# Kernel optimization log

Hardware: AMD Instinct MI355X
Metric: run time of the kernel (lower is better)

The kernel has to match this reference:

```python
import jax, jax.numpy as jnp
import numpy as np

B, S, D, H = 32, 2048, 128, 16  # batch, cached kv len, head dim (=d_model), heads
EPS = 1e-5


def setup_inputs() -> dict:
    key = jax.random.key(0)
    ks = jax.random.split(key, 5)
    d_total = D * H
    x = jax.random.normal(ks[0], (B, 1, D), jnp.float32)
    past_k = jax.random.normal(ks[1], (B, H, S, D), jnp.float32)
    past_v = jax.random.normal(ks[2], (B, H, S, D), jnp.float32)
    Wqkv = jax.random.normal(ks[3], (3 * d_total, D), jnp.float32) * 0.02
    bqkv = jnp.zeros((3 * d_total,), jnp.float32)
    Wout = jax.random.normal(ks[4], (D, d_total), jnp.float32) * 0.02
    bout = jnp.zeros((D,), jnp.float32)
    return {"x": x, "past_k": past_k, "past_v": past_v,
            "Wqkv": Wqkv, "bqkv": bqkv, "Wout": Wout, "bout": bout}


def reference(x, past_k, past_v, Wqkv, bqkv, Wout, bout):
    # QKV projection: (B,1,D) -> (B,1,3*H*D)
    qkv = x @ Wqkv.T + bqkv
    qkv = qkv.reshape(B, 1, 3 * H, D).transpose(0, 2, 1, 3)  # (B,3H,1,D)
    q, k_new, v_new = jnp.split(qkv, 3, axis=1)              # each (B,H,1,D)
    k = jnp.concatenate([past_k, k_new], axis=2)             # (B,H,S+1,D)
    v = jnp.concatenate([past_v, v_new], axis=2)
    # single-query attention (causal mask is trivially all-visible for q_len=1)
    scale = 1.0 / jnp.sqrt(jnp.float32(D))
    scores = jnp.einsum('bhqd,bhkd->bhqk', q, k) * scale     # (B,H,1,S+1)
    probs = jax.nn.softmax(scores, axis=-1)
    y = jnp.einsum('bhqk,bhkd->bhqd', probs, v)              # (B,H,1,D)
    y = y.transpose(0, 2, 1, 3).reshape(B, 1, H * D)         # (B,1,H*D)
    y = y @ Wout.T + bout                                    # (B,1,D)
    y = y + x                                                # residual
    # layer norm over last dim, no affine params
    mu = jnp.mean(y, axis=-1, keepdims=True)
    var = jnp.mean(jnp.square(y - mu), axis=-1, keepdims=True)
    out = (y - mu) / jnp.sqrt(var + EPS)
    return (out, k, v)
```

## Files before the change

### kernel.cpp

```cpp
#include <hip/hip_runtime.h>
#include <math.h>

#define B 32
#define S 2048
#define S1 2049
#define D 128
#define H 16
#define DT 2048
#define NS 4
#define ROWS_PER_SPLIT 512
#define EPS 1e-5f
#define SCALE 0.08838834764831845f

typedef float f4v __attribute__((ext_vector_type(4)));

__global__ void __launch_bounds__(256)
qkv_proj_kernel(const float* __restrict__ x,
                const float* __restrict__ Wqkv,
                const float* __restrict__ bqkv,
                float* __restrict__ qkv,
                float* __restrict__ out_k,
                float* __restrict__ out_v) {
    const int b = blockIdx.x;
    const int j = blockIdx.y * 256 + threadIdx.x;
    __shared__ float xs[D];
    if (threadIdx.x < D) xs[threadIdx.x] = x[b * D + threadIdx.x];
    __syncthreads();
    const float* w = Wqkv + (size_t)j * D;
    float acc = bqkv[j];
#pragma unroll
    for (int d = 0; d < D; d += 4) {
        float4 w4 = *reinterpret_cast<const float4*>(w + d);
        acc = fmaf(w4.x, xs[d + 0], acc);
        acc = fmaf(w4.y, xs[d + 1], acc);
        acc = fmaf(w4.z, xs[d + 2], acc);
        acc = fmaf(w4.w, xs[d + 3], acc);
    }
    qkv[(size_t)b * (3 * DT) + j] = acc;

    if (j >= DT) {
        const int r = j - DT;
        const int which = r >> 11;
        const int hd = r & (DT - 1);
        const int h = hd >> 7;
        const int d = hd & 127;
        float* dst = which ? out_v : out_k;
        dst[((size_t)(b * H + h) * S1 + S) * D + d] = acc;
    }
}

__global__ void __launch_bounds__(256)
attn_kernel(const float* __restrict__ past_k,
            const float* __restrict__ past_v,
            const float* __restrict__ qkv,
            float* __restrict__ out_k,
            float* __restrict__ out_v,
            float* __restrict__ part_ml,
            float* __restrict__ part_acc) {
    const int bx = blockIdx.x;
    const int split = bx & (NS - 1);
    const int bh = bx >> 2;
    const int b = bh >> 4;
    const int h = bh & (H - 1);
    const int tid  = threadIdx.x;
    const int wave = tid >> 6;
    const int lane = tid & 63;
    const int half = lane >> 5;
    const int l32  = lane & 31;
    const int rg   = wave * 2 + half;

    const f4v* __restrict__ kin  = (const f4v*)past_k + (size_t)(b * H + h) * S * 32;
    const f4v* __restrict__ vin  = (const f4v*)past_v + (size_t)(b * H + h) * S * 32;
    f4v* __restrict__ kout = (f4v*)out_k + (size_t)(b * H + h) * S1 * 32;
    f4v* __restrict__ vout = (f4v*)out_v + (size_t)(b * H + h) * S1 * 32;

    const f4v q4 = ((const f4v*)qkv)[(size_t)b * (3 * DT / 4) + h * 32 + l32];

    const int s0 = split * ROWS_PER_SPLIT + rg;

    float m = -1e30f;
    float l = 0.f;
    f4v acc = (f4v){0.f, 0.f, 0.f, 0.f};

#pragma unroll 4
    for (int it = 0; it < ROWS_PER_SPLIT / 8; ++it) {
        const int s = s0 + it * 8;
        const size_t off = (size_t)s * 32 + l32;
        f4v k4 = __builtin_nontemporal_load(&kin[off]);
        __builtin_nontemporal_store(k4, &kout[off]);
        f4v t = k4 * q4;
        float p = t.x + t.y + t.z + t.w;
        p += __shfl_xor(p, 1);
        p += __shfl_xor(p, 2);
        p += __shfl_xor(p, 4);
        p += __shfl_xor(p, 8);
        p += __shfl_xor(p, 16);
        p *= SCALE;
        f4v v4 = __builtin_nontemporal_load(&vin[off]);
        __builtin_nontemporal_store(v4, &vout[off]);
        const float mn = fmaxf(m, p);
        const float c = __expf(m - mn);
        const float e = __expf(p - mn);
        l = l * c + e;
        acc = acc * c;
        acc += v4 * e;
        m = mn;
    }

    __shared__ float sm[8];
    __shared__ float sl[8];
    __shared__ float sacc[8 * D];
    ((f4v*)sacc)[rg * 32 + l32] = acc;
    if (l32 == 0) { sm[rg] = m; sl[rg] = l; }
    __syncthreads();

    if (tid < D) {
        float M = sm[0];
#pragma unroll
        for (int g = 1; g < 8; ++g) M = fmaxf(M, sm[g]);
        float L = 0.f, y = 0.f;
#pragma unroll
        for (int g = 0; g < 8; ++g) {
            const float wgt = __expf(sm[g] - M);
            L += wgt * sl[g];
            y = fmaf(wgt, sacc[g * D + tid], y);
        }
        part_acc[(size_t)bx * D + tid] = y;
        if (tid == 0) {
            part_ml[2 * bx + 0] = M;
            part_ml[2 * bx + 1] = L;
        }
    }
}

__global__ void __launch_bounds__(1024)
out_proj_kernel(const float* __restrict__ x,
                const float* __restrict__ qkv,
                const float* __restrict__ part_ml,
                const float* __restrict__ part_acc,
                const float* __restrict__ Wout,
                const float* __restrict__ bout,
                float* __restrict__ out) {
    const int b = blockIdx.x;
    const int t = threadIdx.x;
    __shared__ float ys[DT];
    __shared__ float pp[D * 8];
    __shared__ float tb[D];

    {
        const int h = t >> 6;
        const int lane = t & 63;
        const float* qp   = qkv + (size_t)b * (3 * DT) + h * D;
        const float* knew = qp + DT;
        const float* vnew = qp + 2 * DT;
        float pd = qp[2 * lane] * knew[2 * lane] + qp[2 * lane + 1] * knew[2 * lane + 1];
        pd += __shfl_xor(pd, 1);
        pd += __shfl_xor(pd, 2);
        pd += __shfl_xor(pd, 4);
        pd += __shfl_xor(pd, 8);
        pd += __shfl_xor(pd, 16);
        pd += __shfl_xor(pd, 32);
        const float s = pd * SCALE;

        const int bh = b * H + h;
        float m0 = part_ml[2 * (bh * NS + 0)], l0 = part_ml[2 * (bh * NS + 0) + 1];
        float m1 = part_ml[2 * (bh * NS + 1)], l1 = part_ml[2 * (bh * NS + 1) + 1];
        float m2 = part_ml[2 * (bh * NS + 2)], l2 = part_ml[2 * (bh * NS + 2) + 1];
        float m3 = part_ml[2 * (bh * NS + 3)], l3 = part_ml[2 * (bh * NS + 3) + 1];
        float M = fmaxf(fmaxf(fmaxf(m0, m1), fmaxf(m2, m3)), s);
        const float w0 = __expf(m0 - M), w1 = __expf(m1 - M);
        const float w2 = __expf(m2 - M), w3 = __expf(m3 - M);
        const float wn = __expf(s - M);
        const float L = w0 * l0 + w1 * l1 + w2 * l2 + w3 * l3 + wn;
        const float invL = 1.0f / L;
#pragma unroll
        for (int r = 0; r < 2; ++r) {
            const int d = lane + r * 64;
            float y = wn * vnew[d];
            y = fmaf(w0, part_acc[(size_t)(bh * NS + 0) * D + d], y);
            y = fmaf(w1, part_acc[(size_t)(bh * NS + 1) * D + d], y);
            y = fmaf(w2, part_acc[(size_t)(bh * NS + 2) * D + d], y);
            y = fmaf(w3, part_acc[(size_t)(bh * NS + 3) * D + d], y);
            ys[h * D + d] = y * invL;
        }
    }
    __syncthreads();

    {
        const int d = t >> 3;
        const int sub = t & 7;
        const float* w = Wout + (size_t)d * DT + sub * 256;
        const float* y = ys + sub * 256;
        float acc = 0.f;
#pragma unroll
        for (int j = 0; j < 256; j += 4) {
            float4 w4 = *reinterpret_cast<const float4*>(w + j);
            acc = fmaf(w4.x, y[j + 0], acc);
            acc = fmaf(w4.y, y[j + 1], acc);
            acc = fmaf(w4.z, y[j + 2], acc);
            acc = fmaf(w4.w, y[j + 3], acc);
        }
        pp[d * 8 + sub] = acc;
    }
    __syncthreads();

    float val = 0.f;
    if (t < D) {
        float a = 0.f;
#pragma unroll
        for (int g = 0; g < 8; ++g) a += pp[t * 8 + g];
        val = a + bout[t] + x[b * D + t];
        tb[t] = val;
    }
    __syncthreads();
    for (int off = 64; off > 0; off >>= 1) {
        if (t < off) tb[t] += tb[t + off];
        __syncthreads();
    }
    const float mu = tb[0] * (1.0f / D);
    __syncthreads();
    const float diff = val - mu;
    if (t < D) tb[t] = diff * diff;
    __syncthreads();
    for (int off = 64; off > 0; off >>= 1) {
        if (t < off) tb[t] += tb[t + off];
        __syncthreads();
    }
    const float var = tb[0] * (1.0f / D);
    if (t < D) out[(size_t)b * D + t] = diff / sqrtf(var + EPS);
}

extern "C" void kernel_launch(void* const* d_in, const int* in_sizes, int n_in,
                              void* d_out, int out_size, void* d_ws, size_t ws_size,
                              hipStream_t stream) {
    const float* x      = (const float*)d_in[0];
    const float* past_k = (const float*)d_in[1];
    const float* past_v = (const float*)d_in[2];
    const float* Wqkv   = (const float*)d_in[3];
    const float* bqkv   = (const float*)d_in[4];
    const float* Wout   = (const float*)d_in[5];
    const float* bout   = (const float*)d_in[6];

    float* out   = (float*)d_out;
    float* out_k = out + (size_t)B * D;
    float* out_v = out_k + (size_t)B * H * S1 * D;

    float* qkv      = (float*)d_ws;
    float* part_ml  = qkv + (size_t)B * 3 * DT;
    float* part_acc = part_ml + 2 * B * H * NS;

    qkv_proj_kernel<<<dim3(B, (3 * DT) / 256), 256, 0, stream>>>(
        x, Wqkv, bqkv, qkv, out_k, out_v);
    attn_kernel<<<B * H * NS, 256, 0, stream>>>(
        past_k, past_v, qkv, out_k, out_v, part_ml, part_acc);
    out_proj_kernel<<<B, 1024, 0, stream>>>(
        x, qkv, part_ml, part_acc, Wout, bout, out);
}
```

Baseline: 493.9 us.

## Split attention into two-pass score/softmax then V accumulation per split

Replaces the per-row online softmax in the attention kernel with two passes. The first streams K and writes scaled scores to shared memory. A block-wide max and sum-of-exponentials reduction follows, then a second pass streams V and accumulates with the precomputed weights. This removes the per-row rescaling exps and multiplies from the dependent V loop, and the final merge across row groups becomes a plain sum. In exchange it adds extra barriers and separates the K and V streams, which may reduce memory-level parallelism in a bandwidth-bound kernel.

```diff
diff --git a/kernel.cpp b/kernel.cpp
--- a/kernel.cpp
+++ b/kernel.cpp
@@ -8,7 +8,7 @@
 #define H 16
 #define DT 2048
 #define NS 4
-#define ROWS_PER_SPLIT 512
+#define RPS 512
 #define EPS 1e-5f
 #define SCALE 0.08838834764831845f
 
@@ -69,6 +69,11 @@
     const int l32  = lane & 31;
     const int rg   = wave * 2 + half;
 
+    __shared__ float sc[RPS];
+    __shared__ float swm[4];
+    __shared__ float swl[4];
+    __shared__ float sacc[8 * D];
+
     const f4v* __restrict__ kin  = (const f4v*)past_k + (size_t)(b * H + h) * S * 32;
     const f4v* __restrict__ vin  = (const f4v*)past_v + (size_t)(b * H + h) * S * 32;
     f4v* __restrict__ kout = (f4v*)out_k + (size_t)(b * H + h) * S1 * 32;
@@ -76,16 +81,12 @@
 
     const f4v q4 = ((const f4v*)qkv)[(size_t)b * (3 * DT / 4) + h * 32 + l32];
 
-    const int s0 = split * ROWS_PER_SPLIT + rg;
-
-    float m = -1e30f;
-    float l = 0.f;
-    f4v acc = (f4v){0.f, 0.f, 0.f, 0.f};
-
-#pragma unroll 4
-    for (int it = 0; it < ROWS_PER_SPLIT / 8; ++it) {
-        const int s = s0 + it * 8;
-        const size_t off = (size_t)s * 32 + l32;
+    const size_t base = (size_t)split * RPS * 32;
+
+#pragma unroll 8
+    for (int it = 0; it < RPS / 8; ++it) {
+        const int r = it * 8 + rg;
+        const size_t off = base + (size_t)r * 32 + l32;
         f4v k4 = __builtin_nontemporal_load(&kin[off]);
         __builtin_nontemporal_store(k4, &kout[off]);
         f4v t = k4 * q4;
@@ -95,36 +96,47 @@
         p += __shfl_xor(p, 4);
         p += __shfl_xor(p, 8);
         p += __shfl_xor(p, 16);
-        p *= SCALE;
+        if (l32 == 0) sc[r] = p * SCALE;
+    }
+    __syncthreads();
+
+    float s0v = sc[tid];
+    float s1v = sc[tid + 256];
+    float m = fmaxf(s0v, s1v);
+#pragma unroll
+    for (int off = 1; off < 64; off <<= 1) m = fmaxf(m, __shfl_xor(m, off));
+    if (lane == 0) swm[wave] = m;
+    __syncthreads();
+    const float M = fmaxf(fmaxf(swm[0], swm[1]), fmaxf(swm[2], swm[3]));
+    const float e0 = __expf(s0v - M);
+    const float e1 = __expf(s1v - M);
+    sc[tid] = e0;
+    sc[tid + 256] = e1;
+    float lsum = e0 + e1;
+#pragma unroll
+    for (int off = 1; off < 64; off <<= 1) lsum += __shfl_xor(lsum, off);
+    if (lane == 0) swl[wave] = lsum;
+    __syncthreads();
+    const float L = swl[0] + swl[1] + swl[2] + swl[3];
+
+    f4v acc = (f4v){0.f, 0.f, 0.f, 0.f};
+#pragma unroll 8
+    for (int it = 0; it < RPS / 8; ++it) {
+        const int r = it * 8 + rg;
+        const size_t off = base + (size_t)r * 32 + l32;
         f4v v4 = __builtin_nontemporal_load(&vin[off]);
         __builtin_nontemporal_store(v4, &vout[off]);
-        const float mn = fmaxf(m, p);
-        const float c = __expf(m - mn);
-        const float e = __expf(p - mn);
-        l = l * c + e;
-        acc = acc * c;
-        acc += v4 * e;
-        m = mn;
-    }
-
-    __shared__ float sm[8];
-    __shared__ float sl[8];
-    __shared__ float sacc[8 * D];
+        const float p = sc[r];
+        acc += v4 * p;
+    }
+
     ((f4v*)sacc)[rg * 32 + l32] = acc;
-    if (l32 == 0) { sm[rg] = m; sl[rg] = l; }
     __syncthreads();
 
     if (tid < D) {
-        float M = sm[0];
-#pragma unroll
-        for (int g = 1; g < 8; ++g) M = fmaxf(M, sm[g]);
-        float L = 0.f, y = 0.f;
-#pragma unroll
-        for (int g = 0; g < 8; ++g) {
-            const float wgt = __expf(sm[g] - M);
-            L += wgt * sl[g];
-            y = fmaf(wgt, sacc[g * D + tid], y);
-        }
+        float y = 0.f;
+#pragma unroll
+        for (int g = 0; g < 8; ++g) y += sacc[g * D + tid];
         part_acc[(size_t)bx * D + tid] = y;
         if (tid == 0) {
             part_ml[2 * bx + 0] = M;
```

Result: faster. 468.8 us (-5.1%).
